# Optimization experiments

Hardware: AMD Instinct MI355X
Metric: run time of the kernel (lower is better)

Reference implementation:

```python
import jax, jax.numpy as jnp
import numpy as np

EMB = 1024
HEADS = 16
HEAD_DIM = EMB // HEADS


def setup_inputs() -> dict:
    key = jax.random.key(0)
    ks = jax.random.split(key, 5)
    x = jax.random.normal(ks[0], (2, 2048, EMB), dtype=jnp.float32)
    # per-head projection params, stacked over heads: [H, E, D]
    Wq = jax.random.normal(ks[1], (HEADS, EMB, HEAD_DIM), dtype=jnp.float32)
    Wk = jax.random.normal(ks[2], (HEADS, EMB, HEAD_DIM), dtype=jnp.float32)
    Wv = jax.random.normal(ks[3], (HEADS, EMB, HEAD_DIM), dtype=jnp.float32)
    # output projection (torch Linear weight [out, in], bias=False)
    Wo = jax.random.normal(ks[4], (EMB, EMB), dtype=jnp.float32) * (1.0 / np.sqrt(EMB))
    return {"x": x, "Wq": Wq, "Wk": Wk, "Wv": Wv, "Wo": Wo}


def reference(x, Wq, Wk, Wv, Wo):
    B, T, E = x.shape
    # per-head projections: [B, H, T, D]
    q = jnp.einsum('bte,hed->bhtd', x, Wq)
    k = jnp.einsum('bte,hed->bhtd', x, Wk)
    v = jnp.einsum('bte,hed->bhtd', x, Wv)
    scale = 1.0 / jnp.sqrt(jnp.asarray(HEAD_DIM, dtype=x.dtype))
    scores = jnp.einsum('bhtd,bhsd->bhts', q, k) * scale  # [B,H,T,T]
    s = jax.nn.softmax(scores, axis=-1)
    out = jnp.einsum('bhts,bhsd->bhtd', s, v)
    # concat heads along last dim in head order: [B, T, H*D]
    combined = jnp.transpose(out, (0, 2, 1, 3)).reshape(B, T, E)
    # residual + output projection (Linear bias=False: y = combined @ Wo.T)
    return x + combined @ Wo.T
```

## Files before the change

### kernel.cpp

```cpp
#include <hip/hip_runtime.h>

#define EMB   1024
#define HEADS 16
#define HDIM  64
#define BATCH 2
#define SEQ   2048
#define MROWS (BATCH*SEQ)
#define STR   40
#define QSCALE 0.1803368801111204f

typedef __attribute__((ext_vector_type(8))) short bf16x8;
typedef __attribute__((ext_vector_type(4))) float f32x4;
typedef __attribute__((ext_vector_type(16))) float f32x16;
typedef unsigned short u16;

__device__ __forceinline__ u16 f2bf(float f) {
    unsigned u = __float_as_uint(f);
    u += 0x7fffu + ((u >> 16) & 1u);
    return (u16)(u >> 16);
}
__device__ __forceinline__ float bf2f(u16 h) {
    return __uint_as_float((unsigned)h << 16);
}
__device__ __forceinline__ float fast_exp2(float x) {
#if __has_builtin(__builtin_amdgcn_exp2f)
    return __builtin_amdgcn_exp2f(x);
#else
    return __expf(x * 0.6931471805599453f);
#endif
}
__device__ __forceinline__ unsigned pk_trunc(float lo, float hi) {
    return __builtin_amdgcn_perm(__float_as_uint(hi), __float_as_uint(lo),
                                 0x07060302u);
}
__device__ __forceinline__ void gload16(const u16* g, u16* l) {
    __builtin_amdgcn_global_load_lds(
        (const __attribute__((address_space(1))) unsigned int*)g,
        (__attribute__((address_space(3))) unsigned int*)l, 16, 0, 0);
}

#define SWZ(r, ch) ((((r) << 6)) + ((((ch) ^ ((r) & 7))) << 3))

__global__ __launch_bounds__(256)
void prep1(const float* __restrict__ X, const float* __restrict__ Wq,
           const float* __restrict__ Wk, const float* __restrict__ Wv,
           u16* __restrict__ Xh, u16* __restrict__ Xl,
           u16* __restrict__ Qth, u16* __restrict__ Qtl,
           u16* __restrict__ Kth, u16* __restrict__ Ktl,
           u16* __restrict__ Vth)
{
    const int bx = blockIdx.x;
    if (bx < 2048) {
        int i = (bx * 256 + threadIdx.x) * 8;
#pragma unroll
        for (int half = 0; half < 2; ++half) {
            float4 v = *(const float4*)(X + i + half * 4);
            ushort4 hi, lo;
            hi.x = f2bf(v.x); lo.x = f2bf(v.x - bf2f(hi.x));
            hi.y = f2bf(v.y); lo.y = f2bf(v.y - bf2f(hi.y));
            hi.z = f2bf(v.z); lo.z = f2bf(v.z - bf2f(hi.z));
            hi.w = f2bf(v.w); lo.w = f2bf(v.w - bf2f(hi.w));
            *(ushort4*)(Xh + i + half * 4) = hi;
            *(ushort4*)(Xl + i + half * 4) = lo;
        }
    } else if (bx < 3072) {
        const int f = bx - 2048;
        const int z = f >> 9, y = (f >> 5) & 15, x = f & 31;
        const float* W  = z ? Wk  : Wq;
        u16* Oh         = z ? Kth : Qth;
        u16* Ol         = z ? Ktl : Qtl;
        const int d  = threadIdx.x & 63;
        const int e0 = (x * 4 + (threadIdx.x >> 6)) * 8;
        const float* src = W + ((size_t)y * EMB + e0) * HDIM + d;
        ushort4 h0, h1, l0, l1;
        float v; u16 hv;
        v = src[0 * 64]; hv = f2bf(v); h0.x = hv; l0.x = f2bf(v - bf2f(hv));
        v = src[1 * 64]; hv = f2bf(v); h0.y = hv; l0.y = f2bf(v - bf2f(hv));
        v = src[2 * 64]; hv = f2bf(v); h0.z = hv; l0.z = f2bf(v - bf2f(hv));
        v = src[3 * 64]; hv = f2bf(v); h0.w = hv; l0.w = f2bf(v - bf2f(hv));
        v = src[4 * 64]; hv = f2bf(v); h1.x = hv; l1.x = f2bf(v - bf2f(hv));
        v = src[5 * 64]; hv = f2bf(v); h1.y = hv; l1.y = f2bf(v - bf2f(hv));
        v = src[6 * 64]; hv = f2bf(v); h1.z = hv; l1.z = f2bf(v - bf2f(hv));
        v = src[7 * 64]; hv = f2bf(v); h1.w = hv; l1.w = f2bf(v - bf2f(hv));
        size_t obase = ((size_t)y * HDIM + d) * EMB + e0;
        *(ushort4*)(Oh + obase)     = h0;
        *(ushort4*)(Oh + obase + 4) = h1;
        *(ushort4*)(Ol + obase)     = l0;
        *(ushort4*)(Ol + obase + 4) = l1;
    } else {
        const int f = bx - 3072;
        const int y = f >> 5, x = f & 31;
        const int d  = threadIdx.x & 63;
        const int e0 = (x * 4 + (threadIdx.x >> 6)) * 8;
        const float* src = Wv + ((size_t)y * EMB + e0) * HDIM + d;
        ushort4 h0, h1;
        h0.x = f2bf(src[0 * 64]); h0.y = f2bf(src[1 * 64]);
        h0.z = f2bf(src[2 * 64]); h0.w = f2bf(src[3 * 64]);
        h1.x = f2bf(src[4 * 64]); h1.y = f2bf(src[5 * 64]);
        h1.z = f2bf(src[6 * 64]); h1.w = f2bf(src[7 * 64]);
        size_t obase = ((size_t)y * HDIM + d) * EMB + e0;
        *(ushort4*)(Vth + obase)     = h0;
        *(ushort4*)(Vth + obase + 4) = h1;
    }
}

__global__ __launch_bounds__(256, 2)
void qkv_fused(const u16* __restrict__ Xh, const u16* __restrict__ Xl,
               const u16* __restrict__ Wqh, const u16* __restrict__ Wql,
               const u16* __restrict__ Wkh, const u16* __restrict__ Wkl,
               const u16* __restrict__ Wvt,
               u16* __restrict__ Qh, u16* __restrict__ Ql,
               u16* __restrict__ Kh, u16* __restrict__ Kl,
               u16* __restrict__ Vt)
{
    const int z  = blockIdx.z;
    const bool isV = (z == 2);
    const int m0 = blockIdx.x * 128;
    const int n0 = blockIdx.y * 128;
    const int t    = threadIdx.x;
    const int wave = t >> 6, lane = t & 63;
    const int wm = wave & 1, wn = wave >> 1;
    const int l16 = lane & 15, quad = lane >> 4;

    __shared__ u16 Ahs[128][STR];
    __shared__ u16 Als[128][STR];
    __shared__ u16 Bhs[128][STR];
    __shared__ u16 Bls[128][STR];

    const u16* Bh_g = isV ? Wvt : (z ? Wkh : Wqh);
    const u16* Bl_g = z ? Wkl : Wql;

    const int ar0 = t >> 2, ak = (t & 3) * 8, ar1 = ar0 + 64;

    f32x4 acc[4][4];
#pragma unroll
    for (int i = 0; i < 4; ++i)
#pragma unroll
        for (int j = 0; j < 4; ++j) acc[i][j] = (f32x4){0.f, 0.f, 0.f, 0.f};

    bf16x8 cur[8], nxt[8], nx2[8];
#define QK_LOAD(dst, kk)                                                            \
    do {                                                                            \
        dst[0] = *(const bf16x8*)(Xh  + (size_t)(m0 + ar0) * EMB + (kk) + ak);      \
        dst[1] = *(const bf16x8*)(Xh  + (size_t)(m0 + ar1) * EMB + (kk) + ak);      \
        dst[4] = *(const bf16x8*)(Bh_g + (size_t)(n0 + ar0) * EMB + (kk) + ak);     \
        dst[5] = *(const bf16x8*)(Bh_g + (size_t)(n0 + ar1) * EMB + (kk) + ak);     \
        if (!isV) {                                                                 \
            dst[2] = *(const bf16x8*)(Xl  + (size_t)(m0 + ar0) * EMB + (kk) + ak);  \
            dst[3] = *(const bf16x8*)(Xl  + (size_t)(m0 + ar1) * EMB + (kk) + ak);  \
            dst[6] = *(const bf16x8*)(Bl_g + (size_t)(n0 + ar0) * EMB + (kk) + ak); \
            dst[7] = *(const bf16x8*)(Bl_g + (size_t)(n0 + ar1) * EMB + (kk) + ak); \
        }                                                                           \
    } while (0)

    QK_LOAD(cur, 0);
    QK_LOAD(nxt, 32);

    for (int k0 = 0; k0 < EMB; k0 += 32) {
        __syncthreads();
        *(bf16x8*)&Ahs[ar0][ak] = cur[0];  *(bf16x8*)&Ahs[ar1][ak] = cur[1];
        *(bf16x8*)&Bhs[ar0][ak] = cur[4];  *(bf16x8*)&Bhs[ar1][ak] = cur[5];
        if (!isV) {
            *(bf16x8*)&Als[ar0][ak] = cur[2];  *(bf16x8*)&Als[ar1][ak] = cur[3];
            *(bf16x8*)&Bls[ar0][ak] = cur[6];  *(bf16x8*)&Bls[ar1][ak] = cur[7];
        }
        __syncthreads();

        const int kn = (k0 + 64 < EMB) ? k0 + 64 : 0;
        QK_LOAD(nx2, kn);

        bf16x8 B4h[4], B4l[4];
#pragma unroll
        for (int j = 0; j < 4; ++j) {
            B4h[j] = *(const bf16x8*)&Bhs[wn * 64 + 16 * j + l16][quad * 8];
            if (!isV)
                B4l[j] = *(const bf16x8*)&Bls[wn * 64 + 16 * j + l16][quad * 8];
        }
#pragma unroll
        for (int i = 0; i < 4; ++i) {
            bf16x8 Ai_h = *(const bf16x8*)&Ahs[wm * 64 + 16 * i + l16][quad * 8];
            if (!isV) {
                bf16x8 Ai_l = *(const bf16x8*)&Als[wm * 64 + 16 * i + l16][quad * 8];
#pragma unroll
                for (int j = 0; j < 4; ++j) {
                    acc[i][j] = __builtin_amdgcn_mfma_f32_16x16x32_bf16(Ai_h, B4h[j], acc[i][j], 0, 0, 0);
                    acc[i][j] = __builtin_amdgcn_mfma_f32_16x16x32_bf16(Ai_h, B4l[j], acc[i][j], 0, 0, 0);
                    acc[i][j] = __builtin_amdgcn_mfma_f32_16x16x32_bf16(Ai_l, B4h[j], acc[i][j], 0, 0, 0);
                }
            } else {
#pragma unroll
                for (int j = 0; j < 4; ++j)
                    acc[i][j] = __builtin_amdgcn_mfma_f32_16x16x32_bf16(Ai_h, B4h[j], acc[i][j], 0, 0, 0);
            }
        }
#pragma unroll
        for (int q = 0; q < 8; ++q) { cur[q] = nxt[q]; nxt[q] = nx2[q]; }
    }
#undef QK_LOAD

    const int b = m0 >> 11;
    const int h = (n0 + wn * 64) >> 6;
    if (isV) {
#pragma unroll
        for (int i = 0; i < 4; ++i)
#pragma unroll
            for (int j = 0; j < 4; ++j) {
                int d  = 16 * j + l16;
                int tt = (m0 & (SEQ - 1)) + wm * 64 + 16 * i + quad * 4;
                ushort4 o;
                o.x = f2bf(acc[i][j][0]); o.y = f2bf(acc[i][j][1]);
                o.z = f2bf(acc[i][j][2]); o.w = f2bf(acc[i][j][3]);
                *(ushort4*)(Vt + ((size_t)(b * HEADS + h) * HDIM + d) * SEQ + tt) = o;
            }
    } else {
        u16* Oh = z ? Kh : Qh;
        u16* Ol = z ? Kl : Ql;
        const float esc = z ? 1.0f : QSCALE;
#pragma unroll
        for (int i = 0; i < 4; ++i)
#pragma unroll
            for (int r = 0; r < 4; ++r) {
                int tt = (m0 & (SEQ - 1)) + wm * 64 + 16 * i + quad * 4 + r;
                size_t rowbase = ((size_t)(b * HEADS + h) * SEQ + tt) * HDIM;
#pragma unroll
                for (int j = 0; j < 4; ++j) {
                    int d = 16 * j + l16;
                    float v = acc[i][j][r] * esc;
                    u16 hv = f2bf(v);
                    Oh[rowbase + d] = hv;
                    Ol[rowbase + d] = f2bf(v - bf2f(hv));
                }
            }
    }
}

__global__ __launch_bounds__(256, 3)
void attn_mfma(const u16* __restrict__ Qh, const u16* __restrict__ Ql,
               const u16* __restrict__ Kh, const u16* __restrict__ Kl,
               const u16* __restrict__ Vt, u16* __restrict__ Cb,
               const float* __restrict__ Wo, u16* __restrict__ Woh)
{
    const int w = blockIdx.x;
    if (w >= 1024) {
        int base = ((w - 1024) * 256 + threadIdx.x) * 8;
#pragma unroll 4
        for (int it = 0; it < 32; ++it) {
#pragma unroll
            for (int half = 0; half < 2; ++half) {
                float4 v = *(const float4*)(Wo + base + half * 4);
                ushort4 o;
                o.x = f2bf(v.x); o.y = f2bf(v.y); o.z = f2bf(v.z); o.w = f2bf(v.w);
                *(ushort4*)(Woh + base + half * 4) = o;
            }
            base += 16 * 256 * 8;
        }
        return;
    }

    const int g     = w >> 3;
    const int qtile = g & 31;
    const int bh    = (w & 7) + ((g >> 5) << 3);

    const int t    = threadIdx.x;
    const int wave = t >> 6;
    const int lane = t & 63;
    const int l31  = lane & 31;
    const int hi   = lane >> 5;
    const int wq   = wave & 1;
    const int wk   = wave >> 1;

    __shared__ u16 lds[24576];

    const size_t bh_off = (size_t)bh * SEQ * HDIM;
    const u16* Qhb = Qh + bh_off;
    const u16* Qlb = Ql + bh_off;
    const u16* Khb = Kh + bh_off;
    const u16* Klb = Kl + bh_off;
    const u16* Vtb = Vt + bh_off;

    const int qb0 = qtile * 64 + wq * 32;

    bf16x8 bQh[4], bQl[4];
#pragma unroll
    for (int ks = 0; ks < 4; ++ks) {
        const u16* pH = Qhb + (size_t)(qb0 + l31) * HDIM + ks * 16 + hi * 8;
        const u16* pL = Qlb + (size_t)(qb0 + l31) * HDIM + ks * 16 + hi * 8;
        bQh[ks] = *(const bf16x8*)pH;
        bQl[ks] = *(const bf16x8*)pL;
    }

    f32x16 accO0, accO1;
#pragma unroll
    for (int r = 0; r < 16; ++r) { accO0[r] = 0.f; accO1[r] = 0.f; }
    float m_i = -1e30f, l_i = 0.f;

    const int r8  = lane >> 3;
    const int cSw = (lane & 7) ^ (r8 & 7);
    const int rowA = wave * 16 + r8;
    const size_t koffA = (size_t)rowA * HDIM + cSw * 8;
    const size_t koffB = koffA + 8 * HDIM;
    const size_t voffA = (size_t)rowA * SEQ + cSw * 8;
    const size_t voffB = voffA + (size_t)8 * SEQ;

#define STAGE(b, s0_)                                                              \
    do { const int bb = (b) * 12288; const int wb = bb + wave * 1024;              \
        gload16(Khb + (size_t)(s0_) * HDIM + koffA, &lds[wb]);                     \
        gload16(Khb + (size_t)(s0_) * HDIM + koffB, &lds[wb + 512]);               \
        gload16(Klb + (size_t)(s0_) * HDIM + koffA, &lds[wb + 4096]);              \
        gload16(Klb + (size_t)(s0_) * HDIM + koffB, &lds[wb + 4096 + 512]);        \
        gload16(Vtb + (s0_) + voffA,                &lds[wb + 8192]);              \
        gload16(Vtb + (s0_) + voffB,                &lds[wb + 8192 + 512]);        \
    } while (0)

    STAGE(0, 0);
    __syncthreads();

    const int l7 = lane & 7;
    for (int it = 0; it < 32; ++it) {
        const int cur = it & 1;
        if (it < 31) STAGE(cur ^ 1, (it + 1) * 64);

        const u16* KhL = &lds[cur * 12288];
        const u16* KlL = KhL + 4096;
        const u16* VL  = KhL + 8192;

        f32x16 accS;
#pragma unroll
        for (int r = 0; r < 16; ++r) accS[r] = 0.f;
        __builtin_amdgcn_s_setprio(1);
#pragma unroll
        for (int ks = 0; ks < 4; ++ks) {
            const int off = (wk * 32 + l31) * 64 + (((2 * ks + hi) ^ l7)) * 8;
            bf16x8 kh = *(const bf16x8*)(KhL + off);
            bf16x8 kl = *(const bf16x8*)(KlL + off);
            accS = __builtin_amdgcn_mfma_f32_32x32x16_bf16(kh, bQh[ks], accS, 0, 0, 0);
            accS = __builtin_amdgcn_mfma_f32_32x32x16_bf16(kl, bQh[ks], accS, 0, 0, 0);
            accS = __builtin_amdgcn_mfma_f32_32x32x16_bf16(kh, bQl[ks], accS, 0, 0, 0);
        }
        __builtin_amdgcn_s_setprio(0);

        float P[16];
        {
            float vmax = fmaxf(fmaxf(accS[0], accS[1]), fmaxf(accS[2], accS[3]));
#pragma unroll
            for (int r = 4; r < 16; r += 4)
                vmax = fmaxf(vmax, fmaxf(fmaxf(accS[r], accS[r + 1]),
                                         fmaxf(accS[r + 2], accS[r + 3])));
            vmax = fmaxf(vmax, __shfl_xor(vmax, 32, 64));
            if (!__all(vmax - m_i <= 8.0f)) {
                float mn = fmaxf(m_i, vmax);
                float alph = fast_exp2(m_i - mn);
                m_i = mn;
                l_i *= alph;
#pragma unroll
                for (int r = 0; r < 16; ++r) { accO0[r] *= alph; accO1[r] *= alph; }
            }
            float s = 0.f;
#pragma unroll
            for (int r = 0; r < 16; ++r) {
                P[r] = fast_exp2(accS[r] - m_i);
                s += P[r];
            }
            s += __shfl_xor(s, 32, 64);
            l_i += s;
        }

        unsigned A_[4], B_[4];
#pragma unroll
        for (int rq = 0; rq < 4; ++rq) {
            A_[rq] = pk_trunc(P[4 * rq + 0], P[4 * rq + 1]);
            B_[rq] = pk_trunc(P[4 * rq + 2], P[4 * rq + 3]);
        }
        bf16x8 bP[2];
#pragma unroll
        for (int ks = 0; ks < 2; ++ks) {
            unsigned sndA = hi ? A_[2 * ks] : A_[2 * ks + 1];
            unsigned sndB = hi ? B_[2 * ks] : B_[2 * ks + 1];
            unsigned rcvA = __shfl_xor(sndA, 32, 64);
            unsigned rcvB = __shfl_xor(sndB, 32, 64);
            union { unsigned u[4]; bf16x8 v; } tmp;
            tmp.u[0] = hi ? rcvA : A_[2 * ks];
            tmp.u[1] = hi ? rcvB : B_[2 * ks];
            tmp.u[2] = hi ? A_[2 * ks + 1] : rcvA;
            tmp.u[3] = hi ? B_[2 * ks + 1] : rcvB;
            bP[ks] = tmp.v;
        }

        __builtin_amdgcn_s_setprio(1);
#pragma unroll
        for (int ks = 0; ks < 2; ++ks) {
            const int c0 = (4 * wk + 2 * ks + hi);
            bf16x8 v0 = *(const bf16x8*)(VL + l31 * 64        + ((c0 ^ l7)) * 8);
            bf16x8 v1 = *(const bf16x8*)(VL + (32 + l31) * 64 + ((c0 ^ l7)) * 8);
            accO0 = __builtin_amdgcn_mfma_f32_32x32x16_bf16(v0, bP[ks], accO0, 0, 0, 0);
            accO1 = __builtin_amdgcn_mfma_f32_32x32x16_bf16(v1, bP[ks], accO1, 0, 0, 0);
        }
        __builtin_amdgcn_s_setprio(0);

        __syncthreads();
    }
#undef STAGE

    float* fb = (float*)lds;
    const int slot = (wave * 64 + lane) * 34;
#pragma unroll
    for (int r = 0; r < 16; ++r) {
        fb[slot + r]      = accO0[r];
        fb[slot + 16 + r] = accO1[r];
    }
    fb[slot + 32] = m_i;
    fb[slot + 33] = l_i;
    __syncthreads();
    if (wk == 0) {
        const int ps = ((wave + 2) * 64 + lane) * 34;
        const float m1 = fb[ps + 32], l1 = fb[ps + 33];
        const float mS = fmaxf(m_i, m1);
        float f0 = fast_exp2(m_i - mS);
        float f1 = fast_exp2(m1 - mS);
        const float inv = 1.f / (l_i * f0 + l1 * f1);
        f0 *= inv; f1 *= inv;
        const int b = bh >> 4, h = bh & 15;
        u16* crow = Cb + ((size_t)b * SEQ + qb0 + l31) * EMB + h * HDIM;
#pragma unroll
        for (int rq = 0; rq < 4; ++rq) {
            ushort4 o;
            o.x = f2bf(accO0[4 * rq + 0] * f0 + fb[ps + 4 * rq + 0] * f1);
            o.y = f2bf(accO0[4 * rq + 1] * f0 + fb[ps + 4 * rq + 1] * f1);
            o.z = f2bf(accO0[4 * rq + 2] * f0 + fb[ps + 4 * rq + 2] * f1);
            o.w = f2bf(accO0[4 * rq + 3] * f0 + fb[ps + 4 * rq + 3] * f1);
            *(ushort4*)(crow + 8 * rq + 4 * hi) = o;
        }
#pragma unroll
        for (int rq = 0; rq < 4; ++rq) {
            ushort4 o;
            o.x = f2bf(accO1[4 * rq + 0] * f0 + fb[ps + 16 + 4 * rq + 0] * f1);
            o.y = f2bf(accO1[4 * rq + 1] * f0 + fb[ps + 16 + 4 * rq + 1] * f1);
            o.z = f2bf(accO1[4 * rq + 2] * f0 + fb[ps + 16 + 4 * rq + 2] * f1);
            o.w = f2bf(accO1[4 * rq + 3] * f0 + fb[ps + 16 + 4 * rq + 3] * f1);
            *(ushort4*)(crow + 32 + 8 * rq + 4 * hi) = o;
        }
    }
}

__global__ __launch_bounds__(256, 2)
void oproj_mfma(const u16* __restrict__ Cb, const u16* __restrict__ Woh,
                const float* __restrict__ X, float* __restrict__ Y)
{
    const int m0 = blockIdx.x * 64;
    const int n0 = blockIdx.y * 128;
    const int t    = threadIdx.x;
    const int wave = t >> 6, lane = t & 63;
    const int wm = wave & 1, wn = wave >> 1;
    const int l16 = lane & 15, quad = lane >> 4;

    __shared__ u16 Ahs[64][STR];
    __shared__ u16 Bhs[128][STR];

    const int ar0 = t >> 2, ak = (t & 3) * 8, ar1 = ar0 + 64;

    f32x4 acc[2][4];
#pragma unroll
    for (int i = 0; i < 2; ++i)
#pragma unroll
        for (int j = 0; j < 4; ++j) acc[i][j] = (f32x4){0.f, 0.f, 0.f, 0.f};

    bf16x8 cur[3], nxt[3], nx2[3];
#define O_LOAD(dst, kk)                                                         \
    do {                                                                        \
        dst[0] = *(const bf16x8*)(Cb  + (size_t)(m0 + ar0) * EMB + (kk) + ak);  \
        dst[1] = *(const bf16x8*)(Woh + (size_t)(n0 + ar0) * EMB + (kk) + ak);  \
        dst[2] = *(const bf16x8*)(Woh + (size_t)(n0 + ar1) * EMB + (kk) + ak);  \
    } while (0)

    O_LOAD(cur, 0);
    O_LOAD(nxt, 32);

    for (int k0 = 0; k0 < EMB; k0 += 32) {
        __syncthreads();
        *(bf16x8*)&Ahs[ar0][ak] = cur[0];
        *(bf16x8*)&Bhs[ar0][ak] = cur[1];  *(bf16x8*)&Bhs[ar1][ak] = cur[2];
        __syncthreads();

        const int kn = (k0 + 64 < EMB) ? k0 + 64 : 0;
        O_LOAD(nx2, kn);

        bf16x8 B4[4];
#pragma unroll
        for (int j = 0; j < 4; ++j)
            B4[j] = *(const bf16x8*)&Bhs[wn * 64 + 16 * j + l16][quad * 8];
#pragma unroll
        for (int i = 0; i < 2; ++i) {
            bf16x8 Ai = *(const bf16x8*)&Ahs[wm * 32 + 16 * i + l16][quad * 8];
#pragma unroll
            for (int j = 0; j < 4; ++j)
                acc[i][j] = __builtin_amdgcn_mfma_f32_16x16x32_bf16(Ai, B4[j], acc[i][j], 0, 0, 0);
        }
#pragma unroll
        for (int q = 0; q < 3; ++q) { cur[q] = nxt[q]; nxt[q] = nx2[q]; }
    }
#undef O_LOAD

#pragma unroll
    for (int i = 0; i < 2; ++i)
#pragma unroll
        for (int r = 0; r < 4; ++r) {
            int m = m0 + wm * 32 + 16 * i + quad * 4 + r;
#pragma unroll
            for (int j = 0; j < 4; ++j) {
                int n = n0 + wn * 64 + 16 * j + l16;
                Y[(size_t)m * EMB + n] = acc[i][j][r] + X[(size_t)m * EMB + n];
            }
        }
}

extern "C" void kernel_launch(void* const* d_in, const int* in_sizes, int n_in,
                              void* d_out, int out_size, void* d_ws,
                              size_t ws_size, hipStream_t stream)
{
    const float* x  = (const float*)d_in[0];
    const float* Wq = (const float*)d_in[1];
    const float* Wk = (const float*)d_in[2];
    const float* Wv = (const float*)d_in[3];
    const float* Wo = (const float*)d_in[4];
    float* Y = (float*)d_out;

    const size_t NPER = (size_t)MROWS * EMB;
    u16* base  = (u16*)d_ws;
    u16* Qh    = base;
    u16* Ql    = Qh + NPER;
    u16* Kh    = Ql + NPER;
    u16* Kl    = Kh + NPER;
    u16* Vt    = Kl + NPER;
    u16* Xh    = Vt + NPER;
    u16* Xl    = Xh + NPER;
    u16* Wtq_h = Xl + NPER;
    u16* Wtq_l = Wtq_h + EMB * EMB;
    u16* Wtk_h = Wtq_l + EMB * EMB;
    u16* Wtk_l = Wtk_h + EMB * EMB;
    u16* Wvt   = (u16*)d_out;
    u16* Cb    = Xh;
    u16* Woh   = Xl;

    prep1<<<dim3(3584), 256, 0, stream>>>(x, Wq, Wk, Wv, Xh, Xl,
                                          Wtq_h, Wtq_l, Wtk_h, Wtk_l, Wvt);
    qkv_fused<<<dim3(32, 8, 3), 256, 0, stream>>>(Xh, Xl, Wtq_h, Wtq_l,
                                                  Wtk_h, Wtk_l, Wvt,
                                                  Qh, Ql, Kh, Kl, Vt);
    attn_mfma<<<dim3(1040), 256, 0, stream>>>(Qh, Ql, Kh, Kl, Vt, Cb, Wo, Woh);
    oproj_mfma<<<dim3(64, 8), 256, 0, stream>>>(Cb, Woh, x, Y);
}
```

Before: 282.2 us.

## Load K/V tiles directly from global into registers instead of LDS staging

The attention kernel drops the double-buffered global-to-LDS staging of K and V and the per-iteration barrier. Each wave now reads its K fragments from global memory straight into registers, prefetching the next tile's K after the QK MFMAs, and loads V fragments at the top of each iteration. LDS is cut to the small buffer used for the final cross-wave merge. This removes LDS traffic and syncs and may raise occupancy, but gives up sharing tiles across waves, so global/L2 traffic per block rises and global-load latency is more exposed.

```diff
diff --git a/kernel.cpp b/kernel.cpp
--- a/kernel.cpp
+++ b/kernel.cpp
@@ -33,13 +33,6 @@
     return __builtin_amdgcn_perm(__float_as_uint(hi), __float_as_uint(lo),
                                  0x07060302u);
 }
-__device__ __forceinline__ void gload16(const u16* g, u16* l) {
-    __builtin_amdgcn_global_load_lds(
-        (const __attribute__((address_space(1))) unsigned int*)g,
-        (__attribute__((address_space(3))) unsigned int*)l, 16, 0, 0);
-}
-
-#define SWZ(r, ch) ((((r) << 6)) + ((((ch) ^ ((r) & 7))) << 3))
 
 __global__ __launch_bounds__(256)
 void prep1(const float* __restrict__ X, const float* __restrict__ Wq,
@@ -269,7 +262,7 @@
     const int wq   = wave & 1;
     const int wk   = wave >> 1;
 
-    __shared__ u16 lds[24576];
+    __shared__ float fb[2 * 64 * 34];
 
     const size_t bh_off = (size_t)bh * SEQ * HDIM;
     const u16* Qhb = Qh + bh_off;
@@ -294,35 +287,27 @@
     for (int r = 0; r < 16; ++r) { accO0[r] = 0.f; accO1[r] = 0.f; }
     float m_i = -1e30f, l_i = 0.f;
 
-    const int r8  = lane >> 3;
-    const int cSw = (lane & 7) ^ (r8 & 7);
-    const int rowA = wave * 16 + r8;
-    const size_t koffA = (size_t)rowA * HDIM + cSw * 8;
-    const size_t koffB = koffA + 8 * HDIM;
-    const size_t voffA = (size_t)rowA * SEQ + cSw * 8;
-    const size_t voffB = voffA + (size_t)8 * SEQ;
-
-#define STAGE(b, s0_)                                                              \
-    do { const int bb = (b) * 12288; const int wb = bb + wave * 1024;              \
-        gload16(Khb + (size_t)(s0_) * HDIM + koffA, &lds[wb]);                     \
-        gload16(Khb + (size_t)(s0_) * HDIM + koffB, &lds[wb + 512]);               \
-        gload16(Klb + (size_t)(s0_) * HDIM + koffA, &lds[wb + 4096]);              \
-        gload16(Klb + (size_t)(s0_) * HDIM + koffB, &lds[wb + 4096 + 512]);        \
-        gload16(Vtb + (s0_) + voffA,                &lds[wb + 8192]);              \
-        gload16(Vtb + (s0_) + voffB,                &lds[wb + 8192 + 512]);        \
-    } while (0)
-
-    STAGE(0, 0);
-    __syncthreads();
-
-    const int l7 = lane & 7;
+    const u16* pKh = Khb + (size_t)(wk * 32 + l31) * HDIM + hi * 8;
+    const u16* pKl = Klb + (size_t)(wk * 32 + l31) * HDIM + hi * 8;
+    const u16* pV0 = Vtb + (size_t)l31 * SEQ        + (4 * wk + hi) * 8;
+    const u16* pV1 = Vtb + (size_t)(32 + l31) * SEQ + (4 * wk + hi) * 8;
+
+    bf16x8 kh[4], kl[4];
+#pragma unroll
+    for (int ks = 0; ks < 4; ++ks) {
+        kh[ks] = *(const bf16x8*)(pKh + ks * 16);
+        kl[ks] = *(const bf16x8*)(pKl + ks * 16);
+    }
+
     for (int it = 0; it < 32; ++it) {
-        const int cur = it & 1;
-        if (it < 31) STAGE(cur ^ 1, (it + 1) * 64);
-
-        const u16* KhL = &lds[cur * 12288];
-        const u16* KlL = KhL + 4096;
-        const u16* VL  = KhL + 8192;
+        const int s0 = it * 64;
+
+        bf16x8 v0[2], v1[2];
+#pragma unroll
+        for (int ks = 0; ks < 2; ++ks) {
+            v0[ks] = *(const bf16x8*)(pV0 + s0 + ks * 16);
+            v1[ks] = *(const bf16x8*)(pV1 + s0 + ks * 16);
+        }
 
         f32x16 accS;
 #pragma unroll
@@ -330,14 +315,22 @@
         __builtin_amdgcn_s_setprio(1);
 #pragma unroll
         for (int ks = 0; ks < 4; ++ks) {
-            const int off = (wk * 32 + l31) * 64 + (((2 * ks + hi) ^ l7)) * 8;
-            bf16x8 kh = *(const bf16x8*)(KhL + off);
-            bf16x8 kl = *(const bf16x8*)(KlL + off);
-            accS = __builtin_amdgcn_mfma_f32_32x32x16_bf16(kh, bQh[ks], accS, 0, 0, 0);
-            accS = __builtin_amdgcn_mfma_f32_32x32x16_bf16(kl, bQh[ks], accS, 0, 0, 0);
-            accS = __builtin_amdgcn_mfma_f32_32x32x16_bf16(kh, bQl[ks], accS, 0, 0, 0);
+            accS = __builtin_amdgcn_mfma_f32_32x32x16_bf16(kh[ks], bQh[ks], accS, 0, 0, 0);
+            accS = __builtin_amdgcn_mfma_f32_32x32x16_bf16(kl[ks], bQh[ks], accS, 0, 0, 0);
+            accS = __builtin_amdgcn_mfma_f32_32x32x16_bf16(kh[ks], bQl[ks], accS, 0, 0, 0);
         }
         __builtin_amdgcn_s_setprio(0);
+
+        {
+            const int sn = (it < 31) ? s0 + 64 : 0;
+            const u16* nKh = pKh + (size_t)sn * HDIM;
+            const u16* nKl = pKl + (size_t)sn * HDIM;
+#pragma unroll
+            for (int ks = 0; ks < 4; ++ks) {
+                kh[ks] = *(const bf16x8*)(nKh + ks * 16);
+                kl[ks] = *(const bf16x8*)(nKl + ks * 16);
+            }
+        }
 
         float P[16];
         {
@@ -389,30 +382,25 @@
         __builtin_amdgcn_s_setprio(1);
 #pragma unroll
         for (int ks = 0; ks < 2; ++ks) {
-            const int c0 = (4 * wk + 2 * ks + hi);
-            bf16x8 v0 = *(const bf16x8*)(VL + l31 * 64        + ((c0 ^ l7)) * 8);
-            bf16x8 v1 = *(const bf16x8*)(VL + (32 + l31) * 64 + ((c0 ^ l7)) * 8);
-            accO0 = __builtin_amdgcn_mfma_f32_32x32x16_bf16(v0, bP[ks], accO0, 0, 0, 0);
-            accO1 = __builtin_amdgcn_mfma_f32_32x32x16_bf16(v1, bP[ks], accO1, 0, 0, 0);
+            accO0 = __builtin_amdgcn_mfma_f32_32x32x16_bf16(v0[ks], bP[ks], accO0, 0, 0, 0);
+            accO1 = __builtin_amdgcn_mfma_f32_32x32x16_bf16(v1[ks], bP[ks], accO1, 0, 0, 0);
         }
         __builtin_amdgcn_s_setprio(0);
-
-        __syncthreads();
-    }
-#undef STAGE
-
-    float* fb = (float*)lds;
-    const int slot = (wave * 64 + lane) * 34;
-#pragma unroll
-    for (int r = 0; r < 16; ++r) {
-        fb[slot + r]      = accO0[r];
-        fb[slot + 16 + r] = accO1[r];
-    }
-    fb[slot + 32] = m_i;
-    fb[slot + 33] = l_i;
+    }
+
+    if (wk) {
+        const int slot = ((wave - 2) * 64 + lane) * 34;
+#pragma unroll
+        for (int r = 0; r < 16; ++r) {
+            fb[slot + r]      = accO0[r];
+            fb[slot + 16 + r] = accO1[r];
+        }
+        fb[slot + 32] = m_i;
+        fb[slot + 33] = l_i;
+    }
     __syncthreads();
-    if (wk == 0) {
-        const int ps = ((wave + 2) * 64 + lane) * 34;
+    if (!wk) {
+        const int ps = ((wave + 2 - 2) * 64 + lane) * 34;
         const float m1 = fb[ps + 32], l1 = fb[ps + 33];
         const float mS = fmaxf(m_i, m1);
         float f0 = fast_exp2(m_i - mS);
```

Measured after the change: 369.4 us. +30.9%, slower.
